# Performance work log

Measured on AMD Instinct MI355X. Metric: run time of the kernel, lower is better.

## Reference

```python
import math
import jax, jax.numpy as jnp
import numpy as np


def setup_inputs() -> dict:
    key = jax.random.key(0)
    kq, kk, kv, kb, km = jax.random.split(key, 5)
    B, Q, H, C = 2, 2048, 16, 64
    q = jax.random.normal(kq, (B, Q, H, C), jnp.float32)
    k = jax.random.normal(kk, (B, Q, H, C), jnp.float32)
    v = jax.random.normal(kv, (B, Q, H, C), jnp.float32)
    b = jax.random.normal(kb, (B, H, Q, Q), jnp.float32)
    m = jnp.sort(jax.random.randint(km, (B, Q), 0, 4), axis=-1).astype(jnp.int32)
    return {"q": q, "k": k, "v": v, "b": b, "m": m}


def reference(q, k, v, b, m):
    # q,k,v: (B, S, H, C); b: (B, H, S, S); m: (B, S) segment ids (self-attn)
    sm_scale = 1.0 / math.sqrt(q.shape[-1])
    n_q, n_k = q.shape[1], k.shape[1]
    logits = jnp.einsum('bqhc,bkhc->bhqk', q, k).astype(jnp.float32)
    # segment mask: (B, 1, Q, K), True where query/key share a segment id
    seg_mask = (m[:, :, None] == m[:, None, :])[:, None, :, :]
    causal_mask = jnp.tril(jnp.ones((1, 1, n_q, n_k), dtype=bool))
    mask = jnp.logical_and(seg_mask, causal_mask)
    logits = jnp.where(mask, logits, -jnp.inf)
    weights = jax.nn.softmax(logits * sm_scale + b.astype(jnp.float32), axis=-1).astype(q.dtype)
    out = jnp.einsum('bhqk,bkhc->bqhc', weights, v)
    return out.astype(jnp.float32)
```

## Files before the change

### kernel.cpp

```cpp
#include <hip/hip_runtime.h>
#include <hip/hip_bf16.h>
#include <math.h>

#define NB 2
#define SEQ 2048
#define NH 16
#define HD 64
#define QT 64
#define KT 64

typedef short short8 __attribute__((ext_vector_type(8)));
typedef float f32x4 __attribute__((ext_vector_type(4)));
typedef unsigned int u32;
typedef u32 u32x2 __attribute__((ext_vector_type(2)));
typedef u32 u32x4 __attribute__((ext_vector_type(4)));

__device__ __forceinline__ unsigned short f2bf(float f) {
  union { float f; unsigned u; } x; x.f = f;
  unsigned r = x.u + 0x7fffu + ((x.u >> 16) & 1u);
  return (unsigned short)(r >> 16);
}

__device__ __forceinline__ u32 pkbf(float a, float b) {
  u32 r;
  asm("v_cvt_pk_bf16_f32 %0, %1, %2" : "=v"(r) : "v"(a), "v"(b));
  return r;
}

__global__ __launch_bounds__(256, 3) void attn_fwd(
    const float* __restrict__ Qg, const float* __restrict__ Kg,
    const float* __restrict__ Vg, const float* __restrict__ Bg,
    const int* __restrict__ Mg, float* __restrict__ Og)
{
  const int h = blockIdx.x, qt = blockIdx.y, b = blockIdx.z;
  const int q0 = qt * QT;
  const int tid = threadIdx.x;
  const int wave = tid >> 6, lane = tid & 63;
  const int l16 = lane & 15, lhi = lane >> 4;

  __shared__ __align__(16) unsigned short Ks[KT][72];
  __shared__ __align__(16) unsigned short Vt[HD][72];
  __shared__ __align__(16) unsigned short Ps[4][16][72];

  const int* mb = Mg + b * SEQ;
  const int mqf = mb[q0];
  const int mql = mb[q0 + QT - 1];
  int lo = 0, hi = q0 + 1;
  while (lo < hi) { int mid = (lo + hi) >> 1; if (mb[mid] < mqf) lo = mid + 1; else hi = mid; }
  const int k_lo = lo;
  lo = 0; hi = q0 + QT;
  while (lo < hi) { int mid = (lo + hi) >> 1; if (mb[mid] <= mql) lo = mid + 1; else hi = mid; }
  const int k_hi = lo;

  const int kt0 = k_lo & ~(KT - 1);
  const int nt = (k_hi - kt0 + KT - 1) / KT;

  const int qr = q0 + wave * 16;

  const float* qp = Qg + (((size_t)b * SEQ + qr + l16) * NH + h) * HD;
  short8 qf[2];
  #pragma unroll
  for (int s = 0; s < 2; ++s) {
    f32x4 a0 = *(const f32x4*)(qp + lhi * 8 + 32 * s);
    f32x4 a1 = *(const f32x4*)(qp + lhi * 8 + 32 * s + 4);
    short8 t;
    #pragma unroll
    for (int i = 0; i < 4; ++i) {
      t[i]     = (short)f2bf(a0[i] * 0.125f);
      t[i + 4] = (short)f2bf(a1[i] * 0.125f);
    }
    qf[s] = t;
  }

  int mq[4];
  #pragma unroll
  for (int j = 0; j < 4; ++j) mq[j] = mb[qr + lhi * 4 + j];

  f32x4 oacc[4];
  float mrun[4], lrun[4];
  #pragma unroll
  for (int g = 0; g < 4; ++g) { f32x4 z = {0.f, 0.f, 0.f, 0.f}; oacc[g] = z; }
  #pragma unroll
  for (int j = 0; j < 4; ++j) { mrun[j] = -1e30f; lrun[j] = 0.f; }

  const int krow = tid >> 2, kc0 = (tid & 3) * 16;
  const int vkb = (tid >> 4) * 4, vcv = (tid & 15) * 4;
  const size_t rstride = (size_t)NH * HD;
  const float* kbase = Kg + (((size_t)b * SEQ + krow) * NH + h) * HD + kc0;
  const float* vbase = Vg + (((size_t)b * SEQ + vkb) * NH + h) * HD + vcv;
  const size_t bbase = (((size_t)b * NH + h) * SEQ) * (size_t)SEQ;

  f32x4 kx0, kx1, kx2, kx3, vx0, vx1, vx2, vx3;
  {
    const float* kp = kbase + (size_t)kt0 * rstride;
    kx0 = *(const f32x4*)(kp);      kx1 = *(const f32x4*)(kp + 4);
    kx2 = *(const f32x4*)(kp + 8);  kx3 = *(const f32x4*)(kp + 12);
    const float* vp = vbase + (size_t)kt0 * rstride;
    vx0 = *(const f32x4*)(vp);
    vx1 = *(const f32x4*)(vp + rstride);
    vx2 = *(const f32x4*)(vp + 2 * rstride);
    vx3 = *(const f32x4*)(vp + 3 * rstride);
  }

  for (int t = 0; t < nt; ++t) {
    const int k0 = kt0 + t * KT;

    float bv[4][4];
    const float* bp0 = Bg + bbase + (size_t)(qr + lhi * 4) * SEQ + k0 + l16;
    #pragma unroll
    for (int j = 0; j < 4; ++j) {
      #pragma unroll
      for (int g = 0; g < 4; ++g) bv[j][g] = bp0[(size_t)j * SEQ + 16 * g];
    }
    int mk[4];
    #pragma unroll
    for (int g = 0; g < 4; ++g) mk[g] = mb[k0 + l16 + 16 * g];

    __syncthreads();

    {
      u32x4 wa, wb;
      wa[0] = pkbf(kx0[0], kx0[1]); wa[1] = pkbf(kx0[2], kx0[3]);
      wa[2] = pkbf(kx1[0], kx1[1]); wa[3] = pkbf(kx1[2], kx1[3]);
      wb[0] = pkbf(kx2[0], kx2[1]); wb[1] = pkbf(kx2[2], kx2[3]);
      wb[2] = pkbf(kx3[0], kx3[1]); wb[3] = pkbf(kx3[2], kx3[3]);
      *(u32x4*)&Ks[krow][kc0]     = wa;
      *(u32x4*)&Ks[krow][kc0 + 8] = wb;
      #pragma unroll
      for (int cc = 0; cc < 4; ++cc) {
        u32x2 wv;
        wv[0] = pkbf(vx0[cc], vx1[cc]);
        wv[1] = pkbf(vx2[cc], vx3[cc]);
        *(u32x2*)&Vt[vcv + cc][vkb] = wv;
      }
    }

    if (t + 1 < nt) {
      const int kn = k0 + KT;
      const float* kp = kbase + (size_t)kn * rstride;
      kx0 = *(const f32x4*)(kp);      kx1 = *(const f32x4*)(kp + 4);
      kx2 = *(const f32x4*)(kp + 8);  kx3 = *(const f32x4*)(kp + 12);
      const float* vp = vbase + (size_t)kn * rstride;
      vx0 = *(const f32x4*)(vp);
      vx1 = *(const f32x4*)(vp + rstride);
      vx2 = *(const f32x4*)(vp + 2 * rstride);
      vx3 = *(const f32x4*)(vp + 3 * rstride);
    }

    __syncthreads();

    f32x4 sacc[4];
    #pragma unroll
    for (int g = 0; g < 4; ++g) { f32x4 z = {0.f, 0.f, 0.f, 0.f}; sacc[g] = z; }
    #pragma unroll
    for (int s = 0; s < 2; ++s) {
      #pragma unroll
      for (int g = 0; g < 4; ++g) {
        short8 kf = *(const short8*)&Ks[l16 + 16 * g][lhi * 8 + 32 * s];
        sacc[g] = __builtin_amdgcn_mfma_f32_16x16x32_bf16(qf[s], kf, sacc[g], 0, 0, 0);
      }
    }

    float sv[4][4];
    #pragma unroll
    for (int g = 0; g < 4; ++g) {
      const int colk = k0 + l16 + 16 * g;
      #pragma unroll
      for (int j = 0; j < 4; ++j) {
        const int rowq = qr + lhi * 4 + j;
        const bool ok = (mk[g] == mq[j]) && (colk <= rowq);
        sv[g][j] = ok ? (sacc[g][j] + bv[j][g]) : -1e30f;
      }
    }

    float resc[4], mnew[4], rsum[4];
    #pragma unroll
    for (int j = 0; j < 4; ++j) {
      float mx = fmaxf(fmaxf(sv[0][j], sv[1][j]), fmaxf(sv[2][j], sv[3][j]));
      mx = fmaxf(mx, __shfl_xor(mx, 1));
      mx = fmaxf(mx, __shfl_xor(mx, 2));
      mx = fmaxf(mx, __shfl_xor(mx, 4));
      mx = fmaxf(mx, __shfl_xor(mx, 8));
      mnew[j] = fmaxf(mrun[j], mx);
      resc[j] = __expf(mrun[j] - mnew[j]);
      mrun[j] = mnew[j];
      rsum[j] = 0.f;
    }
    float pv[4][4];
    #pragma unroll
    for (int g = 0; g < 4; ++g) {
      #pragma unroll
      for (int j = 0; j < 4; ++j) {
        float p = (sv[g][j] > -9e29f) ? __expf(sv[g][j] - mnew[j]) : 0.f;
        pv[g][j] = p;
        rsum[j] += p;
      }
    }
    #pragma unroll
    for (int j = 0; j < 4; ++j) {
      float r = rsum[j];
      r += __shfl_xor(r, 1); r += __shfl_xor(r, 2);
      r += __shfl_xor(r, 4); r += __shfl_xor(r, 8);
      lrun[j] = lrun[j] * resc[j] + r;
    }
    #pragma unroll
    for (int g = 0; g < 4; ++g) {
      #pragma unroll
      for (int j = 0; j < 4; ++j) oacc[g][j] *= resc[j];
    }

    #pragma unroll
    for (int g = 0; g < 4; ++g) {
      #pragma unroll
      for (int j = 0; j < 4; ++j)
        Ps[wave][lhi * 4 + j][l16 + 16 * g] = (unsigned short)pkbf(pv[g][j], pv[g][j]);
    }

    #pragma unroll
    for (int s = 0; s < 2; ++s) {
      short8 pf = *(const short8*)&Ps[wave][l16][lhi * 8 + 32 * s];
      #pragma unroll
      for (int g = 0; g < 4; ++g) {
        short8 vf = *(const short8*)&Vt[l16 + 16 * g][lhi * 8 + 32 * s];
        oacc[g] = __builtin_amdgcn_mfma_f32_16x16x32_bf16(pf, vf, oacc[g], 0, 0, 0);
      }
    }
  }

  #pragma unroll
  for (int j = 0; j < 4; ++j) {
    const float inv = 1.f / lrun[j];
    float* op = Og + (((size_t)b * SEQ + qr + lhi * 4 + j) * NH + h) * HD + l16;
    #pragma unroll
    for (int g = 0; g < 4; ++g) op[16 * g] = oacc[g][j] * inv;
  }
}

extern "C" void kernel_launch(void* const* d_in, const int* in_sizes, int n_in,
                              void* d_out, int out_size, void* d_ws, size_t ws_size,
                              hipStream_t stream) {
  const float* q = (const float*)d_in[0];
  const float* k = (const float*)d_in[1];
  const float* v = (const float*)d_in[2];
  const float* bias = (const float*)d_in[3];
  const int* m = (const int*)d_in[4];
  float* out = (float*)d_out;

  dim3 grid(NH, SEQ / QT, NB);
  dim3 block(256);
  hipLaunchKernelGGL(attn_fwd, grid, block, 0, stream, q, k, v, bias, m, out);
}
```

Before: 48.35 us.

## Permute K/V rows in LDS so bias and mask load as vectors

K rows are written into LDS in a permuted order, and V columns are transposed to match, so each lane's four score columns map to four consecutive keys. This lets the dominant bias read and the key segment-id read use 16-byte vector loads instead of scattered scalar loads. The P-to-LDS store is also folded into the exp loop, and the score temporaries are dropped. The cost is more complex index arithmetic, and the LDS write pattern for V changes, which may change bank conflicts.

```diff
diff --git a/kernel.cpp b/kernel.cpp
--- a/kernel.cpp
+++ b/kernel.cpp
@@ -11,6 +11,7 @@
 
 typedef short short8 __attribute__((ext_vector_type(8)));
 typedef float f32x4 __attribute__((ext_vector_type(4)));
+typedef int i32x4 __attribute__((ext_vector_type(4)));
 typedef unsigned int u32;
 typedef u32 u32x2 __attribute__((ext_vector_type(2)));
 typedef u32 u32x4 __attribute__((ext_vector_type(4)));
@@ -26,6 +27,7 @@
   asm("v_cvt_pk_bf16_f32 %0, %1, %2" : "=v"(r) : "v"(a), "v"(b));
   return r;
 }
+
 
 __global__ __launch_bounds__(256, 3) void attn_fwd(
     const float* __restrict__ Qg, const float* __restrict__ Kg,
@@ -84,10 +86,14 @@
   for (int j = 0; j < 4; ++j) { mrun[j] = -1e30f; lrun[j] = 0.f; }
 
   const int krow = tid >> 2, kc0 = (tid & 3) * 16;
-  const int vkb = (tid >> 4) * 4, vcv = (tid & 15) * 4;
+  const int kpr  = ((krow & 3) << 4) | (krow >> 2);
+  const int tg   = tid >> 4;
+  const int vcv  = (tid & 15) * 4;
+  const int vr0  = ((tg & 3) << 4) | (tg >> 2);
+  const int vc0  = tg * 4;
   const size_t rstride = (size_t)NH * HD;
   const float* kbase = Kg + (((size_t)b * SEQ + krow) * NH + h) * HD + kc0;
-  const float* vbase = Vg + (((size_t)b * SEQ + vkb) * NH + h) * HD + vcv;
+  const float* vbase = Vg + (((size_t)b * SEQ + vr0) * NH + h) * HD + vcv;
   const size_t bbase = (((size_t)b * NH + h) * SEQ) * (size_t)SEQ;
 
   f32x4 kx0, kx1, kx2, kx3, vx0, vx1, vx2, vx3;
@@ -97,24 +103,19 @@
     kx2 = *(const f32x4*)(kp + 8);  kx3 = *(const f32x4*)(kp + 12);
     const float* vp = vbase + (size_t)kt0 * rstride;
     vx0 = *(const f32x4*)(vp);
-    vx1 = *(const f32x4*)(vp + rstride);
-    vx2 = *(const f32x4*)(vp + 2 * rstride);
-    vx3 = *(const f32x4*)(vp + 3 * rstride);
+    vx1 = *(const f32x4*)(vp + 4 * rstride);
+    vx2 = *(const f32x4*)(vp + 8 * rstride);
+    vx3 = *(const f32x4*)(vp + 12 * rstride);
   }
 
   for (int t = 0; t < nt; ++t) {
     const int k0 = kt0 + t * KT;
 
-    float bv[4][4];
-    const float* bp0 = Bg + bbase + (size_t)(qr + lhi * 4) * SEQ + k0 + l16;
-    #pragma unroll
-    for (int j = 0; j < 4; ++j) {
-      #pragma unroll
-      for (int g = 0; g < 4; ++g) bv[j][g] = bp0[(size_t)j * SEQ + 16 * g];
-    }
-    int mk[4];
-    #pragma unroll
-    for (int g = 0; g < 4; ++g) mk[g] = mb[k0 + l16 + 16 * g];
+    const float* bprow = Bg + bbase + (size_t)(qr + lhi * 4) * SEQ + k0 + 4 * l16;
+    f32x4 bv4[4];
+    #pragma unroll
+    for (int j = 0; j < 4; ++j) bv4[j] = *(const f32x4*)(bprow + (size_t)j * SEQ);
+    const i32x4 mk = *(const i32x4*)&mb[k0 + 4 * l16];
 
     __syncthreads();
 
@@ -124,14 +125,14 @@
       wa[2] = pkbf(kx1[0], kx1[1]); wa[3] = pkbf(kx1[2], kx1[3]);
       wb[0] = pkbf(kx2[0], kx2[1]); wb[1] = pkbf(kx2[2], kx2[3]);
       wb[2] = pkbf(kx3[0], kx3[1]); wb[3] = pkbf(kx3[2], kx3[3]);
-      *(u32x4*)&Ks[krow][kc0]     = wa;
-      *(u32x4*)&Ks[krow][kc0 + 8] = wb;
+      *(u32x4*)&Ks[kpr][kc0]     = wa;
+      *(u32x4*)&Ks[kpr][kc0 + 8] = wb;
       #pragma unroll
       for (int cc = 0; cc < 4; ++cc) {
         u32x2 wv;
         wv[0] = pkbf(vx0[cc], vx1[cc]);
         wv[1] = pkbf(vx2[cc], vx3[cc]);
-        *(u32x2*)&Vt[vcv + cc][vkb] = wv;
+        *(u32x2*)&Vt[vcv + cc][vc0] = wv;
       }
     }
 
@@ -142,9 +143,9 @@
       kx2 = *(const f32x4*)(kp + 8);  kx3 = *(const f32x4*)(kp + 12);
       const float* vp = vbase + (size_t)kn * rstride;
       vx0 = *(const f32x4*)(vp);
-      vx1 = *(const f32x4*)(vp + rstride);
-      vx2 = *(const f32x4*)(vp + 2 * rstride);
-      vx3 = *(const f32x4*)(vp + 3 * rstride);
+      vx1 = *(const f32x4*)(vp + 4 * rstride);
+      vx2 = *(const f32x4*)(vp + 8 * rstride);
+      vx3 = *(const f32x4*)(vp + 12 * rstride);
     }
 
     __syncthreads();
@@ -161,22 +162,21 @@
       }
     }
 
-    float sv[4][4];
+    const int colk = k0 + 4 * l16;
     #pragma unroll
     for (int g = 0; g < 4; ++g) {
-      const int colk = k0 + l16 + 16 * g;
       #pragma unroll
       for (int j = 0; j < 4; ++j) {
         const int rowq = qr + lhi * 4 + j;
-        const bool ok = (mk[g] == mq[j]) && (colk <= rowq);
-        sv[g][j] = ok ? (sacc[g][j] + bv[j][g]) : -1e30f;
+        const bool ok = (mk[g] == mq[j]) && (colk + g <= rowq);
+        sacc[g][j] = ok ? (sacc[g][j] + bv4[j][g]) : -1e30f;
       }
     }
 
     float resc[4], mnew[4], rsum[4];
     #pragma unroll
     for (int j = 0; j < 4; ++j) {
-      float mx = fmaxf(fmaxf(sv[0][j], sv[1][j]), fmaxf(sv[2][j], sv[3][j]));
+      float mx = fmaxf(fmaxf(sacc[0][j], sacc[1][j]), fmaxf(sacc[2][j], sacc[3][j]));
       mx = fmaxf(mx, __shfl_xor(mx, 1));
       mx = fmaxf(mx, __shfl_xor(mx, 2));
       mx = fmaxf(mx, __shfl_xor(mx, 4));
@@ -186,14 +186,13 @@
       mrun[j] = mnew[j];
       rsum[j] = 0.f;
     }
-    float pv[4][4];
     #pragma unroll
     for (int g = 0; g < 4; ++g) {
       #pragma unroll
       for (int j = 0; j < 4; ++j) {
-        float p = (sv[g][j] > -9e29f) ? __expf(sv[g][j] - mnew[j]) : 0.f;
-        pv[g][j] = p;
+        float p = (sacc[g][j] > -9e29f) ? __expf(sacc[g][j] - mnew[j]) : 0.f;
         rsum[j] += p;
+        Ps[wave][lhi * 4 + j][l16 + 16 * g] = (unsigned short)pkbf(p, p);
       }
     }
     #pragma unroll
@@ -207,13 +206,6 @@
     for (int g = 0; g < 4; ++g) {
       #pragma unroll
       for (int j = 0; j < 4; ++j) oacc[g][j] *= resc[j];
-    }
-
-    #pragma unroll
-    for (int g = 0; g < 4; ++g) {
-      #pragma unroll
-      for (int j = 0; j < 4; ++j)
-        Ps[wave][lhi * 4 + j][l16 + 16 * g] = (unsigned short)pkbf(pv[g][j], pv[g][j]);
     }
 
     #pragma unroll
```

After: 48.41 us. No clear change (+0.1%).
